# Kernel tuning notes

Measured on AMD Instinct MI355X. Metric: run time of the kernel, lower is better.

## Reference

```python
import jax, jax.numpy as jnp
import numpy as np

DIM = 512
BLOCK = 64
SPARSITY = 0.9
B, L = 4, 2048
NEG_INF = jnp.float32(-jnp.inf)


def _block_sparse_mask(key, seq_len, block_size, sparsity):
    # mirrors BasicQuantumAttention._get_block_sparse_mask, with diagonal
    # blocks forced on so no softmax row is fully masked (avoids NaNs)
    nb = (seq_len + block_size - 1) // block_size
    blk = jax.random.uniform(key, (nb, nb)) > sparsity
    blk = jnp.tril(blk) | jnp.eye(nb, dtype=bool)
    m = jnp.repeat(jnp.repeat(blk, block_size, axis=0), block_size, axis=1)
    return m[:seq_len, :seq_len]


def setup_inputs() -> dict:
    key = jax.random.key(0)
    ks = jax.random.split(key, 12)
    d = DIM
    inp = {}
    names = ['q_real', 'q_imag', 'k_real', 'k_imag', 'v_real', 'v_imag']
    for i, n in enumerate(names):
        inp[n] = jax.random.normal(ks[i], (B, L, d), dtype=jnp.float32)
    # xavier-ish init for Linear weights (torch Linear: y = x @ W.T + b)
    s6 = (2.0 / (6 * d + 6 * d)) ** 0.5
    s2 = (2.0 / (2 * d + 2 * d)) ** 0.5
    inp['W_qkv'] = jax.random.normal(ks[6], (6 * d, 6 * d), dtype=jnp.float32) * s6
    inp['b_qkv'] = jnp.zeros((6 * d,), dtype=jnp.float32)
    inp['W_out'] = jax.random.normal(ks[7], (2 * d, 2 * d), dtype=jnp.float32) * s2
    inp['b_out'] = jnp.zeros((2 * d,), dtype=jnp.float32)
    # two independent random block-sparse masks (one per stream, as in the
    # original which regenerates the mask inside each _chunk_attention call)
    inp['mask_real'] = _block_sparse_mask(ks[8], L, BLOCK, SPARSITY)
    inp['mask_imag'] = _block_sparse_mask(ks[9], L, BLOCK, SPARSITY)
    return inp


def _masked_attention(q, k, v, mask, scale):
    # q,k,v: [B,L,d]; mask: [L,L] bool (True = keep)
    scores = jnp.einsum('bqd,bkd->bqk', q, k) * scale
    scores = jnp.where(mask[None, :, :], scores, NEG_INF)
    attn = jax.nn.softmax(scores, axis=-1)  # dropout is identity in eval
    return jnp.einsum('bqk,bkd->bqd', attn, v)


def reference(q_real, q_imag, k_real, k_imag, v_real, v_imag,
              W_qkv, b_qkv, W_out, b_out, mask_real, mask_imag):
    d = q_real.shape[-1]
    scale = jnp.asarray(d, q_real.dtype) ** -0.5
    x = jnp.concatenate([q_real, q_imag, k_real, k_imag, v_real, v_imag], axis=-1)
    qkv = x @ W_qkv.T + b_qkv                       # [B,L,6d]
    q_r, q_i, k_r, k_i, v_r, v_i = jnp.split(qkv, 6, axis=-1)
    out_real = _masked_attention(q_r, k_r, v_r, mask_real, scale)
    out_imag = _masked_attention(q_i, k_i, v_i, mask_imag, scale)
    out = jnp.concatenate([out_real, out_imag], axis=-1)  # [B,L,2d]
    out = out @ W_out.T + b_out
    return out[..., :d], out[..., d:]
```

## Files before the change

### kernel.cpp

```cpp
#include <hip/hip_runtime.h>
#include <stdint.h>

typedef __attribute__((ext_vector_type(8))) short short8;
typedef __attribute__((ext_vector_type(4))) float f32x4;

#define DEV __device__ __forceinline__

DEV unsigned short f2bf(float f) {
    unsigned int u = __float_as_uint(f);
    u += 0x7FFFu + ((u >> 16) & 1u);
    return (unsigned short)(u >> 16);
}

DEV void gload_lds16(const void* g, void* l) {
    __builtin_amdgcn_global_load_lds(
        (const __attribute__((address_space(1))) unsigned int*)g,
        (__attribute__((address_space(3))) unsigned int*)l,
        16, 0, 0);
}

__global__ __launch_bounds__(256) void f32_to_bf16_k(
    const float* __restrict__ in, unsigned short* __restrict__ out, int n8) {
    int i = blockIdx.x * 256 + threadIdx.x;
    if (i >= n8) return;
    const float4* src = (const float4*)in + (size_t)i * 2;
    float4 a = src[0], b = src[1];
    short8 o;
    o[0] = f2bf(a.x); o[1] = f2bf(a.y); o[2] = f2bf(a.z); o[3] = f2bf(a.w);
    o[4] = f2bf(b.x); o[5] = f2bf(b.y); o[6] = f2bf(b.z); o[7] = f2bf(b.w);
    *((short8*)out + i) = o;
}

__global__ __launch_bounds__(256) void pack_x_k(
    const float* __restrict__ p0, const float* __restrict__ p1,
    const float* __restrict__ p2, const float* __restrict__ p3,
    const float* __restrict__ p4, const float* __restrict__ p5,
    unsigned short* __restrict__ x) {
    int i = blockIdx.x * 256 + threadIdx.x;
    int e0 = i * 8;
    int m = e0 / 3072;
    int k = e0 - m * 3072;
    int sel = k >> 9;
    const float* src;
    switch (sel) {
        case 0: src = p0; break; case 1: src = p1; break;
        case 2: src = p2; break; case 3: src = p3; break;
        case 4: src = p4; break; default: src = p5; break;
    }
    src += (size_t)m * 512 + (k & 511);
    float4 a = *(const float4*)src;
    float4 b = *(const float4*)(src + 4);
    short8 o;
    o[0] = f2bf(a.x); o[1] = f2bf(a.y); o[2] = f2bf(a.z); o[3] = f2bf(a.w);
    o[4] = f2bf(b.x); o[5] = f2bf(b.y); o[6] = f2bf(b.z); o[7] = f2bf(b.w);
    *(short8*)(x + e0) = o;
}

__global__ void scan_masks_k(const void* mr, const void* mi,
                             int* __restrict__ nact, unsigned char* __restrict__ lists) {
    int blk = blockIdx.x;
    int s = blk >> 5, qb = blk & 31;
    int lane = threadIdx.x;
    const unsigned char* det = (const unsigned char*)mr;
    bool is_byte = det[1] != 0;
    const void* m = s ? mi : mr;
    bool on = false;
    if (lane < 32) {
        size_t off = (size_t)(qb * 64) * 2048 + (size_t)lane * 64;
        on = is_byte ? (((const unsigned char*)m)[off] != 0)
                     : (((const int*)m)[off] != 0);
    }
    unsigned long long mask = __ballot(on);
    if (on) {
        int pos = __popcll(mask & ((1ull << lane) - 1ull));
        lists[blk * 32 + pos] = (unsigned char)lane;
    }
    if (lane == 0) nact[blk] = (int)__popcll(mask);
}


#define MFMA_TILE(mbase)                                                       \
    do {                                                                       \
        _Pragma("unroll")                                                      \
        for (int m_ = 0; m_ < 4; ++m_) {                                       \
            _Pragma("unroll")                                                  \
            for (int n_ = 0; n_ < NF; ++n_)                                    \
                acc[(mbase) + m_][n_] = __builtin_amdgcn_mfma_f32_16x16x32_bf16( \
                    af[m_], bf[n_], acc[(mbase) + m_][n_], 0, 0, 0);           \
        }                                                                      \
    } while (0)

#define PHASE_PRE()                                          \
    __builtin_amdgcn_s_barrier();                            \
    asm volatile("s_waitcnt lgkmcnt(0)" ::: "memory");       \
    __builtin_amdgcn_sched_barrier(0);                       \
    __builtin_amdgcn_s_setprio(1)

#define PHASE_END()                                          \
    __builtin_amdgcn_s_setprio(0);                           \
    __builtin_amdgcn_s_barrier();                            \
    asm volatile("" ::: "memory")

#define WAIT_VN()                                                          \
    do {                                                                   \
        if constexpr (NF == 2) asm volatile("s_waitcnt vmcnt(2)" ::: "memory"); \
        else if constexpr (NF == 3) asm volatile("s_waitcnt vmcnt(3)" ::: "memory"); \
        else asm volatile("s_waitcnt vmcnt(4)" ::: "memory");              \
    } while (0)

#define PHASE_END_VN()                                       \
    __builtin_amdgcn_s_setprio(0);                           \
    WAIT_VN();                                               \
    __builtin_amdgcn_s_barrier();                            \
    asm volatile("" ::: "memory")

template <int MODE, int NF>
__global__ __launch_bounds__(512, 2) void gemm256(
    const unsigned short* __restrict__ A, const unsigned short* __restrict__ B,
    const float* __restrict__ bias, unsigned short* __restrict__ Cb,
    float* __restrict__ Cf, int M, int N, int K, int NBN, int halfN, int half_elems) {
    constexpr int BN = NF * 64;
    __shared__ unsigned short lds[2][16384 + NF * 4096];
    const int tid = threadIdx.x;
    const int wv = tid >> 6, ln = tid & 63;
    const int fr = ln & 15, fo = ln >> 4;
    const int wr = wv >> 2, wc = wv & 3;
    const int cpx = gridDim.x >> 3;
    const int wgid = (blockIdx.x & 7) * cpx + (blockIdx.x >> 3);
    const int bm = wgid / NBN, bn = wgid % NBN;
    const unsigned short* Abase = A + (size_t)(bm * 256) * K;
    const unsigned short* Bbase = B + (size_t)(bn * BN) * K;
    const int NT = K >> 6;
    const int NI = NT >> 1;

    auto stagePair = [&](int buf, int isB, int t) {
        const unsigned short* G = isB ? Bbase : Abase;
        unsigned short* Ld = &lds[buf][isB ? 16384 : 0];
        const int kcol = t * 64;
        const int nch = isB ? NF : 4;
        #pragma unroll
        for (int r2 = 0; r2 < nch; ++r2) {
            int d = r2 * 8192 + wv * 1024 + ln * 16;
            int sw = d ^ (((d >> 7) & 7) << 4);
            int grow = sw >> 7;
            int gcol = (sw & 127) >> 1;
            gload_lds16(G + (size_t)grow * K + kcol + gcol,
                        (char*)Ld + r2 * 8192 + wv * 1024);
        }
    };
    auto readA = [&](int buf, int mh, int ks, short8* dst) {
        #pragma unroll
        for (int m = 0; m < 4; ++m) {
            int row = wr * 128 + mh * 64 + m * 16 + fr;
            int byte = (row * 128 + ks * 64 + fo * 16) ^ ((row & 7) << 4);
            dst[m] = *(const short8*)((const char*)&lds[buf][0] + byte);
        }
    };
    auto readB = [&](int buf, int ks, short8* dst) {
        #pragma unroll
        for (int n = 0; n < NF; ++n) {
            int row = wc * (NF * 16) + n * 16 + fr;
            int byte = (row * 128 + ks * 64 + fo * 16) ^ ((row & 7) << 4);
            dst[n] = *(const short8*)((const char*)&lds[buf][16384] + byte);
        }
    };

    f32x4 acc[8][NF];
    #pragma unroll
    for (int m = 0; m < 8; ++m)
        #pragma unroll
        for (int n = 0; n < NF; ++n) acc[m][n] = f32x4{0.f, 0.f, 0.f, 0.f};

    stagePair(0, 0, 0);
    stagePair(0, 1, 0);
    stagePair(1, 1, 1);
    WAIT_VN();
    __builtin_amdgcn_s_barrier();
    asm volatile("" ::: "memory");

    for (int i = 0; i < NI; ++i) {
        const int t1 = 2 * i + 1;
        const int tn0 = (2 * i + 2) % NT;
        const int tn1 = (2 * i + 3) % NT;
        short8 af[4], bf[4];
        readA(0, 0, 0, af); readB(0, 0, bf);
        stagePair(1, 0, t1);
        PHASE_PRE(); MFMA_TILE(0); PHASE_END();
        readA(0, 1, 0, af);
        PHASE_PRE(); MFMA_TILE(4); PHASE_END();
        readA(0, 0, 1, af); readB(0, 1, bf);
        PHASE_PRE(); MFMA_TILE(0); PHASE_END();
        readA(0, 1, 1, af);
        stagePair(0, 1, tn0);
        PHASE_PRE(); MFMA_TILE(4); PHASE_END_VN();
        readA(1, 0, 0, af); readB(1, 0, bf);
        stagePair(0, 0, tn0);
        PHASE_PRE(); MFMA_TILE(0); PHASE_END();
        readA(1, 1, 0, af);
        PHASE_PRE(); MFMA_TILE(4); PHASE_END();
        readA(1, 0, 1, af); readB(1, 1, bf);
        PHASE_PRE(); MFMA_TILE(0); PHASE_END();
        readA(1, 1, 1, af);
        stagePair(1, 1, tn1);
        PHASE_PRE(); MFMA_TILE(4); PHASE_END_VN();
    }

    #pragma unroll
    for (int mi = 0; mi < 8; ++mi)
        #pragma unroll
        for (int ni = 0; ni < NF; ++ni)
            #pragma unroll
            for (int j = 0; j < 4; ++j) {
                int gr = bm * 256 + wr * 128 + mi * 16 + fo * 4 + j;
                int gc = bn * BN + wc * (NF * 16) + ni * 16 + fr;
                float v = acc[mi][ni][j] + bias[gc];
                if (MODE == 0) {
                    Cb[(size_t)gr * N + gc] = f2bf(v);
                } else {
                    if (gc < halfN) Cf[(size_t)gr * halfN + gc] = v;
                    else Cf[half_elems + (size_t)gr * halfN + (gc - halfN)] = v;
                }
            }
}

__global__ __launch_bounds__(256) void transpose_v_k(
    const unsigned short* __restrict__ qkv, unsigned short* __restrict__ Vt) {
    int idx = blockIdx.x;
    int kt = idx & 31; idx >>= 5;
    int dt = idx & 7;  idx >>= 3;
    int b  = idx & 3;  idx >>= 2;
    int s  = idx;
    __shared__ unsigned short tile[64][65];
    int t = threadIdx.x;
    int r = t >> 2;
    int cs = (t & 3) * 16;
    const unsigned short* src =
        qkv + (size_t)(b * 2048 + kt * 64 + r) * 3072 + 2048 + s * 512 + dt * 64 + cs;
    short8 v0 = *(const short8*)src;
    short8 v1 = *(const short8*)(src + 8);
    #pragma unroll
    for (int i = 0; i < 8; ++i) { tile[r][cs + i] = v0[i]; tile[r][cs + 8 + i] = v1[i]; }
    __syncthreads();
    short8 o0, o1;
    #pragma unroll
    for (int i = 0; i < 8; ++i) { o0[i] = tile[cs + i][r]; o1[i] = tile[cs + 8 + i][r]; }
    unsigned short* dst =
        Vt + (size_t)((s * 4 + b) * 512 + dt * 64 + r) * 2048 + kt * 64 + cs;
    *(short8*)dst = o0;
    *(short8*)(dst + 8) = o1;
}

__global__ __launch_bounds__(64, 2) void attn_k(
    const unsigned short* __restrict__ qkv, const unsigned short* __restrict__ Vt,
    unsigned short* __restrict__ attn, const int* __restrict__ nact,
    const unsigned char* __restrict__ lists) {
    int wg = blockIdx.x;
    int xcd = wg & 7, idx = wg >> 3;
    int b = xcd >> 1, s = xcd & 1;
    int qb = idx >> 3, quarter = (idx >> 1) & 3, dh = idx & 1;
    int lane = threadIdx.x;
    int fr = lane & 15, fo = lane >> 4;
    const float scale = 0.04419417382415922f;
    __shared__ unsigned short Pl[1024];
    unsigned char* Plb = (unsigned char*)&Pl[0];

    int qoff = s * 512, koff = 1024 + s * 512;
    size_t vtbase = (size_t)((s * 4 + b) * 512 + dh * 256) * 2048;
    int mrow = b * 2048 + qb * 64 + quarter * 16;

    const unsigned short* qrow_ptr = qkv + (size_t)(mrow + fr) * 3072 + qoff + fo * 8;

    f32x4 acc[16];
    #pragma unroll
    for (int di = 0; di < 16; ++di) acc[di] = f32x4{0.f, 0.f, 0.f, 0.f};
    float mr[4] = {-1e30f, -1e30f, -1e30f, -1e30f};
    float lr[4] = {0.f, 0.f, 0.f, 0.f};

    int na = nact[s * 32 + qb];
    const unsigned char* lst = lists + (s * 32 + qb) * 32;

    for (int t = 0; t < na; ++t) {
        int kb = lst[t];
        const unsigned short* kbp =
            qkv + (size_t)(b * 2048 + kb * 64 + fr) * 3072 + koff + fo * 8;
        f32x4 sf[4];
        #pragma unroll
        for (int nf = 0; nf < 4; ++nf) sf[nf] = f32x4{0.f, 0.f, 0.f, 0.f};
        #pragma unroll
        for (int h = 0; h < 2; ++h) {
            short8 qh[8];
            #pragma unroll
            for (int kk = 0; kk < 8; ++kk)
                qh[kk] = *(const short8*)(qrow_ptr + (h * 8 + kk) * 32);
            #pragma unroll
            for (int kk = 0; kk < 8; ++kk) {
                int kc = (h * 8 + kk) * 32;
                short8 k0 = *(const short8*)(kbp + kc);
                short8 k1 = *(const short8*)(kbp + (size_t)16 * 3072 + kc);
                short8 k2 = *(const short8*)(kbp + (size_t)32 * 3072 + kc);
                short8 k3 = *(const short8*)(kbp + (size_t)48 * 3072 + kc);
                sf[0] = __builtin_amdgcn_mfma_f32_16x16x32_bf16(qh[kk], k0, sf[0], 0, 0, 0);
                sf[1] = __builtin_amdgcn_mfma_f32_16x16x32_bf16(qh[kk], k1, sf[1], 0, 0, 0);
                sf[2] = __builtin_amdgcn_mfma_f32_16x16x32_bf16(qh[kk], k2, sf[2], 0, 0, 0);
                sf[3] = __builtin_amdgcn_mfma_f32_16x16x32_bf16(qh[kk], k3, sf[3], 0, 0, 0);
            }
        }
        #pragma unroll
        for (int nf = 0; nf < 4; ++nf) sf[nf] *= scale;
        float bm[4], f_[4], rs[4];
        #pragma unroll
        for (int j = 0; j < 4; ++j) {
            float v = fmaxf(fmaxf(sf[0][j], sf[1][j]), fmaxf(sf[2][j], sf[3][j]));
            #pragma unroll
            for (int off = 1; off < 16; off <<= 1) v = fmaxf(v, __shfl_xor(v, off, 64));
            bm[j] = v;
        }
        #pragma unroll
        for (int j = 0; j < 4; ++j) {
            float mn = fmaxf(mr[j], bm[j]);
            f_[j] = __expf(mr[j] - mn);
            mr[j] = mn;
            rs[j] = 0.f;
        }
        #pragma unroll
        for (int nf = 0; nf < 4; ++nf)
            #pragma unroll
            for (int j = 0; j < 4; ++j) {
                float p = __expf(sf[nf][j] - mr[j]);
                sf[nf][j] = p;
                rs[j] += p;
            }
        #pragma unroll
        for (int j = 0; j < 4; ++j) {
            float v = rs[j];
            #pragma unroll
            for (int off = 1; off < 16; off <<= 1) v += __shfl_xor(v, off, 64);
            lr[j] = lr[j] * f_[j] + v;
        }
        #pragma unroll
        for (int di = 0; di < 16; ++di) {
            acc[di][0] *= f_[0]; acc[di][1] *= f_[1];
            acc[di][2] *= f_[2]; acc[di][3] *= f_[3];
        }
        #pragma unroll
        for (int nf = 0; nf < 4; ++nf)
            #pragma unroll
            for (int j = 0; j < 4; ++j) {
                int row = fo * 4 + j, col = nf * 16 + fr;
                int byte = row * 128 + ((col * 2) ^ ((row & 7) << 4));
                *(unsigned short*)(Plb + byte) = f2bf(sf[nf][j]);
            }
        asm volatile("s_waitcnt lgkmcnt(0)" ::: "memory");
        #pragma unroll
        for (int ks = 0; ks < 2; ++ks) {
            int rbyte = fr * 128 + (((ks * 32 + fo * 8) * 2) ^ ((fr & 7) << 4));
            short8 pf = *(const short8*)(Plb + rbyte);
            const unsigned short* vp =
                Vt + vtbase + (size_t)fr * 2048 + kb * 64 + ks * 32 + fo * 8;
            #pragma unroll
            for (int di = 0; di < 16; ++di) {
                short8 vf = *(const short8*)(vp + (size_t)di * 16 * 2048);
                acc[di] = __builtin_amdgcn_mfma_f32_16x16x32_bf16(pf, vf, acc[di], 0, 0, 0);
            }
        }
    }
    float inv[4];
    #pragma unroll
    for (int j = 0; j < 4; ++j) inv[j] = 1.0f / lr[j];
    unsigned short* orow = attn + (size_t)(mrow + fo * 4) * 1024 + s * 512 + dh * 256 + fr;
    #pragma unroll
    for (int di = 0; di < 16; ++di)
        #pragma unroll
        for (int j = 0; j < 4; ++j)
            orow[(size_t)j * 1024 + di * 16] = f2bf(acc[di][j] * inv[j]);
}

extern "C" void kernel_launch(void* const* d_in, const int* in_sizes, int n_in,
                              void* d_out, int out_size, void* d_ws, size_t ws_size,
                              hipStream_t stream) {
    const float* q_r = (const float*)d_in[0];
    const float* q_i = (const float*)d_in[1];
    const float* k_r = (const float*)d_in[2];
    const float* k_i = (const float*)d_in[3];
    const float* v_r = (const float*)d_in[4];
    const float* v_i = (const float*)d_in[5];
    const float* W_qkv = (const float*)d_in[6];
    const float* b_qkv = (const float*)d_in[7];
    const float* W_out = (const float*)d_in[8];
    const float* b_out = (const float*)d_in[9];
    const void* mask_r = d_in[10];
    const void* mask_i = d_in[11];

    char* ws = (char*)d_ws;
    unsigned short* x    = (unsigned short*)(ws);
    unsigned short* Wq   = (unsigned short*)(ws + 50331648);
    unsigned short* qkv  = (unsigned short*)(ws + 69206016);
    unsigned short* Wo   = (unsigned short*)(ws + 119537664);
    int* nact            = (int*)(ws + 121634816);
    unsigned char* lists = (unsigned char*)(ws + 121634816 + 256);
    unsigned short* Vt   = x;
    unsigned short* attn = x + 8388608;

    f32_to_bf16_k<<<4608, 256, 0, stream>>>(W_qkv, Wq, 1179648);
    f32_to_bf16_k<<<512, 256, 0, stream>>>(W_out, Wo, 131072);
    pack_x_k<<<12288, 256, 0, stream>>>(q_r, q_i, k_r, k_i, v_r, v_i, x);
    scan_masks_k<<<64, 64, 0, stream>>>(mask_r, mask_i, nact, lists);
    gemm256<0, 3><<<512, 512, 0, stream>>>(x, Wq, b_qkv, qkv, nullptr,
                                           8192, 3072, 3072, 16, 0, 0);
    transpose_v_k<<<2048, 256, 0, stream>>>(qkv, Vt);
    attn_k<<<2048, 64, 0, stream>>>(qkv, Vt, attn, nact, lists);
    gemm256<1, 2><<<256, 512, 0, stream>>>(attn, Wo, b_out, nullptr, (float*)d_out,
                                           8192, 1024, 1024, 8, 512, 4194304);
}
```

Measured before the change: 474.7 us.

## Simplify GEMM pipeline to full-tile MFMA phases and row-per-block packing

After: 468.9 us. Within noise of the previous version (-1.2%).

```diff
diff --git a/kernel.cpp b/kernel.cpp
--- a/kernel.cpp
+++ b/kernel.cpp
@@ -31,15 +31,14 @@
     *((short8*)out + i) = o;
 }
 
-__global__ __launch_bounds__(256) void pack_x_k(
+__global__ __launch_bounds__(384) void pack_x_k(
     const float* __restrict__ p0, const float* __restrict__ p1,
     const float* __restrict__ p2, const float* __restrict__ p3,
     const float* __restrict__ p4, const float* __restrict__ p5,
     unsigned short* __restrict__ x) {
-    int i = blockIdx.x * 256 + threadIdx.x;
-    int e0 = i * 8;
-    int m = e0 / 3072;
-    int k = e0 - m * 3072;
+    int m = blockIdx.x;
+    int t = threadIdx.x;
+    int k = t * 8;
     int sel = k >> 9;
     const float* src;
     switch (sel) {
@@ -53,7 +52,7 @@
     short8 o;
     o[0] = f2bf(a.x); o[1] = f2bf(a.y); o[2] = f2bf(a.z); o[3] = f2bf(a.w);
     o[4] = f2bf(b.x); o[5] = f2bf(b.y); o[6] = f2bf(b.z); o[7] = f2bf(b.w);
-    *(short8*)(x + e0) = o;
+    *(short8*)(x + (size_t)m * 3072 + k) = o;
 }
 
 __global__ void scan_masks_k(const void* mr, const void* mi,
@@ -79,14 +78,14 @@
 }
 
 
-#define MFMA_TILE(mbase)                                                       \
+#define MFMA_ALL()                                                             \
     do {                                                                       \
         _Pragma("unroll")                                                      \
-        for (int m_ = 0; m_ < 4; ++m_) {                                       \
+        for (int m_ = 0; m_ < 8; ++m_) {                                       \
             _Pragma("unroll")                                                  \
             for (int n_ = 0; n_ < NF; ++n_)                                    \
-                acc[(mbase) + m_][n_] = __builtin_amdgcn_mfma_f32_16x16x32_bf16( \
-                    af[m_], bf[n_], acc[(mbase) + m_][n_], 0, 0, 0);           \
+                acc[m_][n_] = __builtin_amdgcn_mfma_f32_16x16x32_bf16(         \
+                    a8[m_], b8[n_], acc[m_][n_], 0, 0, 0);                     \
         }                                                                      \
     } while (0)
 
@@ -101,16 +100,9 @@
     __builtin_amdgcn_s_barrier();                            \
     asm volatile("" ::: "memory")
 
-#define WAIT_VN()                                                          \
-    do {                                                                   \
-        if constexpr (NF == 2) asm volatile("s_waitcnt vmcnt(2)" ::: "memory"); \
-        else if constexpr (NF == 3) asm volatile("s_waitcnt vmcnt(3)" ::: "memory"); \
-        else asm volatile("s_waitcnt vmcnt(4)" ::: "memory");              \
-    } while (0)
-
-#define PHASE_END_VN()                                       \
+#define PHASE_END_V0()                                       \
     __builtin_amdgcn_s_setprio(0);                           \
-    WAIT_VN();                                               \
+    asm volatile("s_waitcnt vmcnt(0)" ::: "memory");         \
     __builtin_amdgcn_s_barrier();                            \
     asm volatile("" ::: "memory")
 
@@ -133,7 +125,7 @@
     const int NT = K >> 6;
     const int NI = NT >> 1;
 
-    auto stagePair = [&](int buf, int isB, int t) {
+    auto stageHalf = [&](int buf, int isB, int t) {
         const unsigned short* G = isB ? Bbase : Abase;
         unsigned short* Ld = &lds[buf][isB ? 16384 : 0];
         const int kcol = t * 64;
@@ -148,20 +140,18 @@
                         (char*)Ld + r2 * 8192 + wv * 1024);
         }
     };
-    auto readA = [&](int buf, int mh, int ks, short8* dst) {
-        #pragma unroll
-        for (int m = 0; m < 4; ++m) {
-            int row = wr * 128 + mh * 64 + m * 16 + fr;
+    auto readAB = [&](int buf, int ks, short8* a8, short8* b8) {
+        #pragma unroll
+        for (int m = 0; m < 8; ++m) {
+            int row = wr * 128 + m * 16 + fr;
             int byte = (row * 128 + ks * 64 + fo * 16) ^ ((row & 7) << 4);
-            dst[m] = *(const short8*)((const char*)&lds[buf][0] + byte);
-        }
-    };
-    auto readB = [&](int buf, int ks, short8* dst) {
+            a8[m] = *(const short8*)((const char*)&lds[buf][0] + byte);
+        }
         #pragma unroll
         for (int n = 0; n < NF; ++n) {
             int row = wc * (NF * 16) + n * 16 + fr;
             int byte = (row * 128 + ks * 64 + fo * 16) ^ ((row & 7) << 4);
-            dst[n] = *(const short8*)((const char*)&lds[buf][16384] + byte);
+            b8[n] = *(const short8*)((const char*)&lds[buf][16384] + byte);
         }
     };
 
@@ -171,38 +161,28 @@
         #pragma unroll
         for (int n = 0; n < NF; ++n) acc[m][n] = f32x4{0.f, 0.f, 0.f, 0.f};
 
-    stagePair(0, 0, 0);
-    stagePair(0, 1, 0);
-    stagePair(1, 1, 1);
-    WAIT_VN();
+    stageHalf(0, 0, 0);
+    stageHalf(0, 1, 0);
+    asm volatile("s_waitcnt vmcnt(0)" ::: "memory");
     __builtin_amdgcn_s_barrier();
     asm volatile("" ::: "memory");
 
     for (int i = 0; i < NI; ++i) {
         const int t1 = 2 * i + 1;
         const int tn0 = (2 * i + 2) % NT;
-        const int tn1 = (2 * i + 3) % NT;
-        short8 af[4], bf[4];
-        readA(0, 0, 0, af); readB(0, 0, bf);
-        stagePair(1, 0, t1);
-        PHASE_PRE(); MFMA_TILE(0); PHASE_END();
-        readA(0, 1, 0, af);
-        PHASE_PRE(); MFMA_TILE(4); PHASE_END();
-        readA(0, 0, 1, af); readB(0, 1, bf);
-        PHASE_PRE(); MFMA_TILE(0); PHASE_END();
-        readA(0, 1, 1, af);
-        stagePair(0, 1, tn0);
-        PHASE_PRE(); MFMA_TILE(4); PHASE_END_VN();
-        readA(1, 0, 0, af); readB(1, 0, bf);
-        stagePair(0, 0, tn0);
-        PHASE_PRE(); MFMA_TILE(0); PHASE_END();
-        readA(1, 1, 0, af);
-        PHASE_PRE(); MFMA_TILE(4); PHASE_END();
-        readA(1, 0, 1, af); readB(1, 1, bf);
-        PHASE_PRE(); MFMA_TILE(0); PHASE_END();
-        readA(1, 1, 1, af);
-        stagePair(1, 1, tn1);
-        PHASE_PRE(); MFMA_TILE(4); PHASE_END_VN();
+        short8 a8[8], b8[NF];
+        readAB(0, 0, a8, b8);
+        stageHalf(1, 0, t1);
+        PHASE_PRE(); MFMA_ALL(); PHASE_END();
+        readAB(0, 1, a8, b8);
+        stageHalf(1, 1, t1);
+        PHASE_PRE(); MFMA_ALL(); PHASE_END_V0();
+        readAB(1, 0, a8, b8);
+        stageHalf(0, 0, tn0);
+        PHASE_PRE(); MFMA_ALL(); PHASE_END();
+        readAB(1, 1, a8, b8);
+        stageHalf(0, 1, tn0);
+        PHASE_PRE(); MFMA_ALL(); PHASE_END_V0();
     }
 
     #pragma unroll
@@ -403,7 +383,7 @@
 
     f32_to_bf16_k<<<4608, 256, 0, stream>>>(W_qkv, Wq, 1179648);
     f32_to_bf16_k<<<512, 256, 0, stream>>>(W_out, Wo, 131072);
-    pack_x_k<<<12288, 256, 0, stream>>>(q_r, q_i, k_r, k_i, v_r, v_i, x);
+    pack_x_k<<<8192, 384, 0, stream>>>(q_r, q_i, k_r, k_i, v_r, v_i, x);
     scan_masks_k<<<64, 64, 0, stream>>>(mask_r, mask_i, nact, lists);
     gemm256<0, 3><<<512, 512, 0, stream>>>(x, Wq, b_qkv, qkv, nullptr,
                                            8192, 3072, 3072, 16, 0, 0);
```
